# Optimization experiments

Measured on AMD Instinct MI355X. Metric: run time of the kernel, lower is better.

Reference implementation:

```python
import jax, jax.numpy as jnp
import numpy as np

B, C, H, W = 16, 64, 64, 64
MID = max(1, C // 8)


def setup_inputs() -> dict:
    key = jax.random.key(0)
    k1, k2, k3, k4, k5 = jax.random.split(key, 5)
    x = jax.random.normal(k1, (B, C, H, W), dtype=jnp.float32)
    # 1x1 conv weights (spectral-norm conv collapses to a plain [out,in] matrix
    # with a scalar-normalized weight; we use the effective weight directly)
    Wq = jax.random.normal(k2, (MID, C), dtype=jnp.float32) * 0.05
    Wk = jax.random.normal(k3, (MID, C), dtype=jnp.float32) * 0.05
    Wv = jax.random.normal(k4, (C, C), dtype=jnp.float32) * 0.05
    gamma = jax.random.normal(k5, (1,), dtype=jnp.float32) * 0.1
    return {"x": x, "Wq": Wq, "Wk": Wk, "Wv": Wv, "gamma": gamma}


def reference(x, Wq, Wk, Wv, gamma):
    b, c, h, w = x.shape
    n = h * w
    mid = Wq.shape[0]
    xf = x.reshape(b, c, n)                      # [B,C,N]
    q = jnp.einsum('mc,bcn->bnm', Wq, xf)        # [B,N,mid]
    k = jnp.einsum('mc,bcn->bmn', Wk, xf)        # [B,mid,N]
    scale = np.float32(1.0 / np.sqrt(mid))       # torch: / q.size(-1)**0.5, q last dim = mid
    attn = jax.nn.softmax(jnp.einsum('bnm,bmk->bnk', q, k) * scale, axis=-1)  # [B,N,N]
    v = jnp.einsum('oc,bcn->bon', Wv, xf)        # [B,C,N]
    # torch: bmm(v, attn^T) -> out[b,c,j] = sum_n v[b,c,n] * attn[b,j,n]
    out = jnp.einsum('bon,bjn->boj', v, attn).reshape(b, c, h, w)
    return gamma * out + x
```

## Files before the change

### kernel.cpp

```cpp
#include <hip/hip_runtime.h>
#include <hip/hip_bf16.h>

#define BATCH 16
#define CC    64
#define NN    4096
#define MIDD  8

typedef __attribute__((ext_vector_type(8)))  short short8;
typedef __attribute__((ext_vector_type(16))) float f32x16;
typedef __attribute__((ext_vector_type(2)))  int   v2i;

static __device__ __forceinline__ ushort f2bf(float f) {
    return __bfloat16_as_ushort(__float2bfloat16(f));
}

static __device__ __forceinline__ void glds16(const void* g, void* l) {
    __builtin_amdgcn_global_load_lds(
        (const __attribute__((address_space(1))) unsigned int*)g,
        (__attribute__((address_space(3))) unsigned int*)l, 16, 0, 0);
}

static __device__ __forceinline__ unsigned cvt_pk(float lo, float hi) {
    unsigned r;
    asm("v_cvt_pk_bf16_f32 %0, %1, %2" : "=v"(r) : "v"(lo), "v"(hi));
    return r;
}

__global__ __launch_bounds__(256) void proj_kernel(
    const float* __restrict__ x,
    const float* __restrict__ Wq,
    const float* __restrict__ Wk,
    const float* __restrict__ Wv,
    ushort* __restrict__ qtr,
    ushort* __restrict__ ktr,
    ushort* __restrict__ v)
{
    __shared__ unsigned xT[64 * 32];

    int tid = threadIdx.x;
    int b   = blockIdx.x >> 6;
    int n0  = (blockIdx.x & 63) * 64;

    {
        int n  = tid & 63;
        int cp = tid >> 6;
        const float* xb = x + (size_t)b * CC * NN + n0 + n;
#pragma unroll
        for (int rep = 0; rep < 8; ++rep) {
            int c = cp * 2 + rep * 8;
            float a0 = xb[(size_t)c * NN];
            float a1 = xb[(size_t)(c + 1) * NN];
            int dwlog = cp + rep * 4;
            xT[n * 32 + (dwlog ^ (n & 31))] = cvt_pk(a0, a1);
        }
    }

    int wv   = tid >> 6;
    int lane = tid & 63;
    int hi   = lane >> 5;
    int r    = lane & 31;
    int s_   = wv & 1;
    bool hiT = wv >= 2;

    short8 wfa[4], wfb[4];
    if (!hiT) {
        const float* r0 = (r < 8)  ? (Wq + r * 64)
                        : (r < 16) ? (Wk + (r - 8) * 64)
                                   : (Wv + (r - 16) * 64);
        const float* r1 = Wv + (16 + r) * 64;
#pragma unroll
        for (int kc = 0; kc < 4; ++kc) {
            const float4* p0 = (const float4*)(r0 + kc * 16 + hi * 8);
            const float4* p1 = (const float4*)(r1 + kc * 16 + hi * 8);
            float4 a = p0[0], c4 = p0[1];
            float4 e = p1[0], g4 = p1[1];
            union { short8 s8; unsigned u[4]; } wa, wb;
            wa.u[0] = cvt_pk(a.x, a.y);  wa.u[1] = cvt_pk(a.z, a.w);
            wa.u[2] = cvt_pk(c4.x, c4.y); wa.u[3] = cvt_pk(c4.z, c4.w);
            wb.u[0] = cvt_pk(e.x, e.y);  wb.u[1] = cvt_pk(e.z, e.w);
            wb.u[2] = cvt_pk(g4.x, g4.y); wb.u[3] = cvt_pk(g4.z, g4.w);
            wfa[kc] = wa.s8; wfb[kc] = wb.s8;
        }
    } else {
        const float* r2 = Wv + (size_t)(r < 16 ? (48 + r) : 48) * 64;
        short8 z8 = {};
#pragma unroll
        for (int kc = 0; kc < 4; ++kc) {
            const float4* p2 = (const float4*)(r2 + kc * 16 + hi * 8);
            float4 a = p2[0], c4 = p2[1];
            union { short8 s8; unsigned u[4]; } wa;
            wa.u[0] = cvt_pk(a.x, a.y);  wa.u[1] = cvt_pk(a.z, a.w);
            wa.u[2] = cvt_pk(c4.x, c4.y); wa.u[3] = cvt_pk(c4.z, c4.w);
            wfa[kc] = (r < 16) ? wa.s8 : z8;
            wfb[kc] = z8;
        }
    }

    __syncthreads();

    short8 bf[4];
    int nr = s_ * 32 + r;
#pragma unroll
    for (int kc = 0; kc < 4; ++kc) {
        union { short8 s8; unsigned u[4]; } bu;
#pragma unroll
        for (int i = 0; i < 4; ++i) {
            int dwlog = kc * 8 + hi * 4 + i;
            bu.u[i] = xT[nr * 32 + (dwlog ^ r)];
        }
        bf[kc] = bu.s8;
    }

    int ng = n0 + s_ * 32 + r;
    size_t nb = (size_t)b * NN + ng;
    const float SCLQ = 0.35355339059327373f * 1.4426950408889634f;

    if (!hiT) {
        f32x16 acc = {};
#pragma unroll
        for (int kc = 0; kc < 4; ++kc)
            acc = __builtin_amdgcn_mfma_f32_32x32x16_bf16(wfa[kc], bf[kc], acc, 0, 0, 0);
        uint2 qd, kd, zd; zd.x = 0; zd.y = 0;
        qd.x = cvt_pk(acc[0] * SCLQ, acc[1] * SCLQ);
        qd.y = cvt_pk(acc[2] * SCLQ, acc[3] * SCLQ);
        kd.x = cvt_pk(acc[4], acc[5]);
        kd.y = cvt_pk(acc[6], acc[7]);
        *(uint2*)(qtr + nb * 8 + hi * 4) = qd;
        *(uint2*)(ktr + nb * 16 + hi * 4) = kd;
        *(uint2*)(ktr + nb * 16 + 8 + hi * 4) = zd;
#pragma unroll
        for (int reg = 8; reg < 16; ++reg) {
            int ch = (reg & 3) + 8 * ((reg >> 2) - 2) + 4 * hi;
            v[((size_t)b * CC + ch) * NN + ng] = f2bf(acc[reg]);
        }
        f32x16 ac1 = {};
#pragma unroll
        for (int kc = 0; kc < 4; ++kc)
            ac1 = __builtin_amdgcn_mfma_f32_32x32x16_bf16(wfb[kc], bf[kc], ac1, 0, 0, 0);
#pragma unroll
        for (int reg = 0; reg < 16; ++reg) {
            int ch = 16 + (reg & 3) + 8 * (reg >> 2) + 4 * hi;
            v[((size_t)b * CC + ch) * NN + ng] = f2bf(ac1[reg]);
        }
    } else {
        f32x16 acc = {};
#pragma unroll
        for (int kc = 0; kc < 4; ++kc)
            acc = __builtin_amdgcn_mfma_f32_32x32x16_bf16(wfa[kc], bf[kc], acc, 0, 0, 0);
#pragma unroll
        for (int reg = 0; reg < 8; ++reg) {
            int ch = 48 + (reg & 3) + 8 * (reg >> 2) + 4 * hi;
            v[((size_t)b * CC + ch) * NN + ng] = f2bf(acc[reg]);
        }
    }
}

__global__ __launch_bounds__(512, 4) void attn_kernel(
    const ushort* __restrict__ qtr,
    const ushort* __restrict__ ktr,
    const ushort* __restrict__ v,
    const float*  __restrict__ x,
    const float*  __restrict__ gamma,
    float* __restrict__ out)
{
    __shared__ __align__(16) char lds[2 * 3 * 10240];

    int bid = blockIdx.x;
    int wg  = (bid & 7) * 64 + (bid >> 3);
    int b   = wg >> 5;
    int qt  = wg & 31;

    int tid  = threadIdx.x;
    int wv   = tid >> 6;
    int qs   = wv & 3;
    int h    = wv >> 2;
    int lane = tid & 63;
    int hi   = lane >> 5;
    int ql   = lane & 31;
    int q0   = qt * 128 + qs * 32;
    int gt   = tid & 255;

    short8 qf = *(const short8*)(qtr + ((size_t)b * NN + q0 + ql) * 8);
    float  gm = gamma[0];
    short8 zero8 = {};
    if (hi) qf = zero8;
    asm volatile("s_waitcnt vmcnt(0)" ::: "memory");

    const ushort* kbh = ktr + (size_t)b * NN * 16 + (size_t)h * 2048 * 16;
    const ushort* vbh = v   + (size_t)b * CC * NN + h * 2048;

    int oA = gt >> 3, sA = (gt & 7) ^ (oA & 7);
    int oB = oA + 32,  sB = (gt & 7) ^ (oB & 7);
    const ushort* vsrcA = vbh + (size_t)oA * NN + sA * 8;
    const ushort* vsrcB = vbh + (size_t)oB * NN + sB * 8;
    int lk = gt ^ ((gt >> 3) & 7);
    const ushort* ksrc0 = kbh + (size_t)(lk >> 1) * 16 + (lk & 1) * 8;

    char* base = lds + h * 30720;
    int vdA = gt * 16, vdB = (gt + 256) * 16, kd_ = 8192 + gt * 16;
    char* b0 = base;
    char* b1 = base + 10240;
    char* b2 = base + 20480;

    int L0 = ql * 2 + hi;
    int L1 = (32 + ql) * 2 + hi;
    int k0off = 8192 + (L0 ^ ((L0 >> 3) & 7)) * 16;
    int k1off = 8192 + (L1 ^ ((L1 >> 3) & 7)) * 16;

    union { short8 s8; ushort us[8]; } onesu;
#pragma unroll
    for (int i = 0; i < 8; ++i) onesu.us[i] = 0x3F80;
    short8 ones = onesu.s8;

    f32x16 zf   = {};
    f32x16 acc0 = {};
    f32x16 acc1 = {};
    f32x16 accl = {};

    glds16(vsrcA, b0 + vdA); glds16(vsrcB, b0 + vdB);
    if (gt < 128) glds16(ksrc0, b0 + kd_);
    glds16(vsrcA + 64, b1 + vdA); glds16(vsrcB + 64, b1 + vdB);
    if (gt < 128) glds16(ksrc0 + 64 * 16, b1 + kd_);

    for (int t = 0; t < 32; ++t) {
        int k2 = ((t + 2) & 31) * 64;

        __builtin_amdgcn_s_barrier();
        glds16(vsrcA + k2, b2 + vdA);
        glds16(vsrcB + k2, b2 + vdB);
        if (gt < 128) {
            glds16(ksrc0 + (size_t)k2 * 16, b2 + kd_);
            asm volatile("s_waitcnt vmcnt(6)" ::: "memory");
        } else {
            asm volatile("s_waitcnt vmcnt(4)" ::: "memory");
        }
        __builtin_amdgcn_s_barrier();
        __builtin_amdgcn_sched_barrier(0);

#pragma unroll
        for (int c = 0; c < 2; ++c) {
            short8 kf = *(const short8*)(b0 + (c ? k1off : k0off));
            f32x16 s = __builtin_amdgcn_mfma_f32_32x32x16_bf16(kf, qf, zf, 0, 0, 0);

            float p[16];
#pragma unroll
            for (int r = 0; r < 16; ++r) p[r] = __builtin_amdgcn_exp2f(s[r]);

            unsigned u[8];
#pragma unroll
            for (int i = 0; i < 8; ++i) u[i] = cvt_pk(p[2 * i], p[2 * i + 1]);

            v2i r02 = __builtin_amdgcn_permlane32_swap(u[0], u[2], false, false);
            v2i r13 = __builtin_amdgcn_permlane32_swap(u[1], u[3], false, false);
            v2i r46 = __builtin_amdgcn_permlane32_swap(u[4], u[6], false, false);
            v2i r57 = __builtin_amdgcn_permlane32_swap(u[5], u[7], false, false);
            union { short8 s8; int i4[4]; } P0, P1;
            P0.i4[0] = r02.x; P0.i4[1] = r13.x; P0.i4[2] = r02.y; P0.i4[3] = r13.y;
            P1.i4[0] = r46.x; P1.i4[1] = r57.x; P1.i4[2] = r46.y; P1.i4[3] = r57.y;

            int g0 = (ql * 8 + ((c * 4 + hi) ^ (ql & 7))) * 16;
            int g1 = (ql * 8 + ((c * 4 + 2 + hi) ^ (ql & 7))) * 16;
            short8 vA0 = *(const short8*)(b0 + g0);
            short8 vB0 = *(const short8*)(b0 + g0 + 4096);
            short8 vA1 = *(const short8*)(b0 + g1);
            short8 vB1 = *(const short8*)(b0 + g1 + 4096);

            __builtin_amdgcn_s_setprio(1);
            acc0 = __builtin_amdgcn_mfma_f32_32x32x16_bf16(vA0, P0.s8, acc0, 0, 0, 0);
            acc1 = __builtin_amdgcn_mfma_f32_32x32x16_bf16(vB0, P0.s8, acc1, 0, 0, 0);
            accl = __builtin_amdgcn_mfma_f32_32x32x16_bf16(ones, P0.s8, accl, 0, 0, 0);
            acc0 = __builtin_amdgcn_mfma_f32_32x32x16_bf16(vA1, P1.s8, acc0, 0, 0, 0);
            acc1 = __builtin_amdgcn_mfma_f32_32x32x16_bf16(vB1, P1.s8, acc1, 0, 0, 0);
            accl = __builtin_amdgcn_mfma_f32_32x32x16_bf16(ones, P1.s8, accl, 0, 0, 0);
            __builtin_amdgcn_s_setprio(0);
        }

        char* tp = b0; b0 = b1; b1 = b2; b2 = tp;
    }

    asm volatile("s_waitcnt vmcnt(0)" ::: "memory");
    __syncthreads();

    float* cl = (float*)lds;
    if (h == 1) {
#pragma unroll
        for (int r = 0; r < 16; ++r) {
            int ch = (r & 3) + 8 * (r >> 2) + 4 * hi;
            cl[(qs * 64 + ch) * 32 + ql]      = acc0[r];
            cl[(qs * 64 + 32 + ch) * 32 + ql] = acc1[r];
        }
        cl[8192 + qs * 32 + ql] = accl[0];
    }
    __syncthreads();
    if (h == 0) {
        float den = accl[0] + cl[8192 + qs * 32 + ql];
        float inv = gm / den;
#pragma unroll
        for (int r = 0; r < 16; ++r) {
            int ch = (r & 3) + 8 * (r >> 2) + 4 * hi;
            float n0 = acc0[r] + cl[(qs * 64 + ch) * 32 + ql];
            float n1 = acc1[r] + cl[(qs * 64 + 32 + ch) * 32 + ql];
            size_t i0 = ((size_t)(b * CC + ch)) * NN + q0 + ql;
            size_t i1 = i0 + (size_t)32 * NN;
            out[i0] = n0 * inv + x[i0];
            out[i1] = n1 * inv + x[i1];
        }
    }
}

extern "C" void kernel_launch(void* const* d_in, const int* in_sizes, int n_in,
                              void* d_out, int out_size, void* d_ws, size_t ws_size,
                              hipStream_t stream) {
    const float* x     = (const float*)d_in[0];
    const float* Wq    = (const float*)d_in[1];
    const float* Wk    = (const float*)d_in[2];
    const float* Wv    = (const float*)d_in[3];
    const float* gamma = (const float*)d_in[4];
    float* out = (float*)d_out;

    ushort* qtr = (ushort*)d_ws;
    ushort* ktr = qtr + (size_t)BATCH * NN * 8;
    ushort* vws = ktr + (size_t)BATCH * NN * 16;

    proj_kernel<<<dim3((BATCH * NN) / 64), dim3(256), 0, stream>>>(x, Wq, Wk, Wv, qtr, ktr, vws);
    attn_kernel<<<dim3((BATCH * NN) / 128), dim3(512), 0, stream>>>(qtr, ktr, vws, x, gamma, out);
}
```

Baseline: 142.4 us.

## Shrink attention blocks to 64 queries with double buffering; loop projection over two tiles

The attention kernel now uses 256-thread blocks covering 64 queries each, twice as many blocks, and double-buffers K/V in LDS instead of triple-buffering. This cuts LDS per block, which should allow more resident blocks. The cost is that each K/V tile now feeds only 2 query waves per half, so global/L2 traffic for K/V roughly doubles, and the prefetch distance drops to one tile. The projection kernel now processes two 64-column tiles per block, reusing the converted weight fragments and halving its block count.

```diff
diff --git a/kernel.cpp b/kernel.cpp
--- a/kernel.cpp
+++ b/kernel.cpp
@@ -38,22 +38,8 @@
     __shared__ unsigned xT[64 * 32];
 
     int tid = threadIdx.x;
-    int b   = blockIdx.x >> 6;
-    int n0  = (blockIdx.x & 63) * 64;
-
-    {
-        int n  = tid & 63;
-        int cp = tid >> 6;
-        const float* xb = x + (size_t)b * CC * NN + n0 + n;
-#pragma unroll
-        for (int rep = 0; rep < 8; ++rep) {
-            int c = cp * 2 + rep * 8;
-            float a0 = xb[(size_t)c * NN];
-            float a1 = xb[(size_t)(c + 1) * NN];
-            int dwlog = cp + rep * 4;
-            xT[n * 32 + (dwlog ^ (n & 31))] = cvt_pk(a0, a1);
-        }
-    }
+    int b   = blockIdx.x >> 5;
+    int c0  = (blockIdx.x & 31) * 128;
 
     int wv   = tid >> 6;
     int lane = tid & 63;
@@ -96,66 +82,84 @@
         }
     }
 
-    __syncthreads();
-
-    short8 bf[4];
-    int nr = s_ * 32 + r;
-#pragma unroll
-    for (int kc = 0; kc < 4; ++kc) {
-        union { short8 s8; unsigned u[4]; } bu;
-#pragma unroll
-        for (int i = 0; i < 4; ++i) {
-            int dwlog = kc * 8 + hi * 4 + i;
-            bu.u[i] = xT[nr * 32 + (dwlog ^ r)];
-        }
-        bf[kc] = bu.s8;
-    }
-
-    int ng = n0 + s_ * 32 + r;
-    size_t nb = (size_t)b * NN + ng;
+    int ns = tid & 63;
+    int cp = tid >> 6;
     const float SCLQ = 0.35355339059327373f * 1.4426950408889634f;
 
-    if (!hiT) {
-        f32x16 acc = {};
-#pragma unroll
-        for (int kc = 0; kc < 4; ++kc)
-            acc = __builtin_amdgcn_mfma_f32_32x32x16_bf16(wfa[kc], bf[kc], acc, 0, 0, 0);
-        uint2 qd, kd, zd; zd.x = 0; zd.y = 0;
-        qd.x = cvt_pk(acc[0] * SCLQ, acc[1] * SCLQ);
-        qd.y = cvt_pk(acc[2] * SCLQ, acc[3] * SCLQ);
-        kd.x = cvt_pk(acc[4], acc[5]);
-        kd.y = cvt_pk(acc[6], acc[7]);
-        *(uint2*)(qtr + nb * 8 + hi * 4) = qd;
-        *(uint2*)(ktr + nb * 16 + hi * 4) = kd;
-        *(uint2*)(ktr + nb * 16 + 8 + hi * 4) = zd;
-#pragma unroll
-        for (int reg = 8; reg < 16; ++reg) {
-            int ch = (reg & 3) + 8 * ((reg >> 2) - 2) + 4 * hi;
-            v[((size_t)b * CC + ch) * NN + ng] = f2bf(acc[reg]);
-        }
-        f32x16 ac1 = {};
-#pragma unroll
-        for (int kc = 0; kc < 4; ++kc)
-            ac1 = __builtin_amdgcn_mfma_f32_32x32x16_bf16(wfb[kc], bf[kc], ac1, 0, 0, 0);
-#pragma unroll
-        for (int reg = 0; reg < 16; ++reg) {
-            int ch = 16 + (reg & 3) + 8 * (reg >> 2) + 4 * hi;
-            v[((size_t)b * CC + ch) * NN + ng] = f2bf(ac1[reg]);
-        }
-    } else {
-        f32x16 acc = {};
-#pragma unroll
-        for (int kc = 0; kc < 4; ++kc)
-            acc = __builtin_amdgcn_mfma_f32_32x32x16_bf16(wfa[kc], bf[kc], acc, 0, 0, 0);
-#pragma unroll
-        for (int reg = 0; reg < 8; ++reg) {
-            int ch = 48 + (reg & 3) + 8 * (reg >> 2) + 4 * hi;
-            v[((size_t)b * CC + ch) * NN + ng] = f2bf(acc[reg]);
-        }
-    }
-}
-
-__global__ __launch_bounds__(512, 4) void attn_kernel(
+    for (int it = 0; it < 2; ++it) {
+        int n0 = c0 + it * 64;
+        __syncthreads();
+        {
+            const float* xb = x + (size_t)b * CC * NN + n0 + ns;
+#pragma unroll
+            for (int rep = 0; rep < 8; ++rep) {
+                int c = cp * 2 + rep * 8;
+                float a0 = xb[(size_t)c * NN];
+                float a1 = xb[(size_t)(c + 1) * NN];
+                int dwlog = cp + rep * 4;
+                xT[ns * 32 + (dwlog ^ (ns & 31))] = cvt_pk(a0, a1);
+            }
+        }
+        __syncthreads();
+
+        short8 bf[4];
+        int nr = s_ * 32 + r;
+#pragma unroll
+        for (int kc = 0; kc < 4; ++kc) {
+            union { short8 s8; unsigned u[4]; } bu;
+#pragma unroll
+            for (int i = 0; i < 4; ++i) {
+                int dwlog = kc * 8 + hi * 4 + i;
+                bu.u[i] = xT[nr * 32 + (dwlog ^ r)];
+            }
+            bf[kc] = bu.s8;
+        }
+
+        int ng = n0 + s_ * 32 + r;
+        size_t nb = (size_t)b * NN + ng;
+
+        if (!hiT) {
+            f32x16 acc = {};
+#pragma unroll
+            for (int kc = 0; kc < 4; ++kc)
+                acc = __builtin_amdgcn_mfma_f32_32x32x16_bf16(wfa[kc], bf[kc], acc, 0, 0, 0);
+            uint2 qd, kd, zd; zd.x = 0; zd.y = 0;
+            qd.x = cvt_pk(acc[0] * SCLQ, acc[1] * SCLQ);
+            qd.y = cvt_pk(acc[2] * SCLQ, acc[3] * SCLQ);
+            kd.x = cvt_pk(acc[4], acc[5]);
+            kd.y = cvt_pk(acc[6], acc[7]);
+            *(uint2*)(qtr + nb * 8 + hi * 4) = qd;
+            *(uint2*)(ktr + nb * 16 + hi * 4) = kd;
+            *(uint2*)(ktr + nb * 16 + 8 + hi * 4) = zd;
+#pragma unroll
+            for (int reg = 8; reg < 16; ++reg) {
+                int ch = (reg & 3) + 8 * ((reg >> 2) - 2) + 4 * hi;
+                v[((size_t)b * CC + ch) * NN + ng] = f2bf(acc[reg]);
+            }
+            f32x16 ac1 = {};
+#pragma unroll
+            for (int kc = 0; kc < 4; ++kc)
+                ac1 = __builtin_amdgcn_mfma_f32_32x32x16_bf16(wfb[kc], bf[kc], ac1, 0, 0, 0);
+#pragma unroll
+            for (int reg = 0; reg < 16; ++reg) {
+                int ch = 16 + (reg & 3) + 8 * (reg >> 2) + 4 * hi;
+                v[((size_t)b * CC + ch) * NN + ng] = f2bf(ac1[reg]);
+            }
+        } else {
+            f32x16 acc = {};
+#pragma unroll
+            for (int kc = 0; kc < 4; ++kc)
+                acc = __builtin_amdgcn_mfma_f32_32x32x16_bf16(wfa[kc], bf[kc], acc, 0, 0, 0);
+#pragma unroll
+            for (int reg = 0; reg < 8; ++reg) {
+                int ch = 48 + (reg & 3) + 8 * (reg >> 2) + 4 * hi;
+                v[((size_t)b * CC + ch) * NN + ng] = f2bf(acc[reg]);
+            }
+        }
+    }
+}
+
+__global__ __launch_bounds__(256, 4) void attn_kernel(
     const ushort* __restrict__ qtr,
     const ushort* __restrict__ ktr,
     const ushort* __restrict__ v,
@@ -163,22 +167,21 @@
     const float*  __restrict__ gamma,
     float* __restrict__ out)
 {
-    __shared__ __align__(16) char lds[2 * 3 * 10240];
+    __shared__ __align__(16) char lds[2 * 2 * 10240];
 
     int bid = blockIdx.x;
-    int wg  = (bid & 7) * 64 + (bid >> 3);
-    int b   = wg >> 5;
-    int qt  = wg & 31;
+    int wg  = (bid & 7) * 128 + (bid >> 3);
+    int b   = wg >> 6;
+    int qt  = wg & 63;
 
     int tid  = threadIdx.x;
-    int wv   = tid >> 6;
-    int qs   = wv & 3;
-    int h    = wv >> 2;
+    int h    = tid >> 7;
+    int gt   = tid & 127;
+    int qs   = (tid >> 6) & 1;
     int lane = tid & 63;
     int hi   = lane >> 5;
     int ql   = lane & 31;
-    int q0   = qt * 128 + qs * 32;
-    int gt   = tid & 255;
+    int q0   = qt * 64 + qs * 32;
 
     short8 qf = *(const short8*)(qtr + ((size_t)b * NN + q0 + ql) * 8);
     float  gm = gamma[0];
@@ -189,18 +192,23 @@
     const ushort* kbh = ktr + (size_t)b * NN * 16 + (size_t)h * 2048 * 16;
     const ushort* vbh = v   + (size_t)b * CC * NN + h * 2048;
 
-    int oA = gt >> 3, sA = (gt & 7) ^ (oA & 7);
-    int oB = oA + 32,  sB = (gt & 7) ^ (oB & 7);
-    const ushort* vsrcA = vbh + (size_t)oA * NN + sA * 8;
-    const ushort* vsrcB = vbh + (size_t)oB * NN + sB * 8;
+    const ushort* vsrc[4];
+    int vd[4];
+#pragma unroll
+    for (int j = 0; j < 4; ++j) {
+        int g  = gt + j * 128;
+        int o  = g >> 3;
+        int sl = (g & 7) ^ (o & 7);
+        vsrc[j] = vbh + (size_t)o * NN + sl * 8;
+        vd[j]   = g * 16;
+    }
     int lk = gt ^ ((gt >> 3) & 7);
-    const ushort* ksrc0 = kbh + (size_t)(lk >> 1) * 16 + (lk & 1) * 8;
-
-    char* base = lds + h * 30720;
-    int vdA = gt * 16, vdB = (gt + 256) * 16, kd_ = 8192 + gt * 16;
-    char* b0 = base;
-    char* b1 = base + 10240;
-    char* b2 = base + 20480;
+    const ushort* ksrc = kbh + (size_t)(lk >> 1) * 16 + (lk & 1) * 8;
+    int kd = 8192 + gt * 16;
+
+    char* base = lds + h * 20480;
+    char* cur  = base;
+    char* nxt  = base + 10240;
 
     int L0 = ql * 2 + hi;
     int L1 = (32 + ql) * 2 + hi;
@@ -217,29 +225,24 @@
     f32x16 acc1 = {};
     f32x16 accl = {};
 
-    glds16(vsrcA, b0 + vdA); glds16(vsrcB, b0 + vdB);
-    if (gt < 128) glds16(ksrc0, b0 + kd_);
-    glds16(vsrcA + 64, b1 + vdA); glds16(vsrcB + 64, b1 + vdB);
-    if (gt < 128) glds16(ksrc0 + 64 * 16, b1 + kd_);
+#pragma unroll
+    for (int j = 0; j < 4; ++j) glds16(vsrc[j], cur + vd[j]);
+    glds16(ksrc, cur + kd);
 
     for (int t = 0; t < 32; ++t) {
-        int k2 = ((t + 2) & 31) * 64;
+        int k1 = ((t + 1) & 31) * 64;
 
         __builtin_amdgcn_s_barrier();
-        glds16(vsrcA + k2, b2 + vdA);
-        glds16(vsrcB + k2, b2 + vdB);
-        if (gt < 128) {
-            glds16(ksrc0 + (size_t)k2 * 16, b2 + kd_);
-            asm volatile("s_waitcnt vmcnt(6)" ::: "memory");
-        } else {
-            asm volatile("s_waitcnt vmcnt(4)" ::: "memory");
-        }
+#pragma unroll
+        for (int j = 0; j < 4; ++j) glds16(vsrc[j] + k1, nxt + vd[j]);
+        glds16(ksrc + (size_t)k1 * 16, nxt + kd);
+        asm volatile("s_waitcnt vmcnt(5)" ::: "memory");
         __builtin_amdgcn_s_barrier();
         __builtin_amdgcn_sched_barrier(0);
 
 #pragma unroll
         for (int c = 0; c < 2; ++c) {
-            short8 kf = *(const short8*)(b0 + (c ? k1off : k0off));
+            short8 kf = *(const short8*)(cur + (c ? k1off : k0off));
             f32x16 s = __builtin_amdgcn_mfma_f32_32x32x16_bf16(kf, qf, zf, 0, 0, 0);
 
             float p[16];
@@ -260,10 +263,10 @@
 
             int g0 = (ql * 8 + ((c * 4 + hi) ^ (ql & 7))) * 16;
             int g1 = (ql * 8 + ((c * 4 + 2 + hi) ^ (ql & 7))) * 16;
-            short8 vA0 = *(const short8*)(b0 + g0);
-            short8 vB0 = *(const short8*)(b0 + g0 + 4096);
-            short8 vA1 = *(const short8*)(b0 + g1);
-            short8 vB1 = *(const short8*)(b0 + g1 + 4096);
+            short8 vA0 = *(const short8*)(cur + g0);
+            short8 vB0 = *(const short8*)(cur + g0 + 4096);
+            short8 vA1 = *(const short8*)(cur + g1);
+            short8 vB1 = *(const short8*)(cur + g1 + 4096);
 
             __builtin_amdgcn_s_setprio(1);
             acc0 = __builtin_amdgcn_mfma_f32_32x32x16_bf16(vA0, P0.s8, acc0, 0, 0, 0);
@@ -275,7 +278,7 @@
             __builtin_amdgcn_s_setprio(0);
         }
 
-        char* tp = b0; b0 = b1; b1 = b2; b2 = tp;
+        char* tp = cur; cur = nxt; nxt = tp;
     }
 
     asm volatile("s_waitcnt vmcnt(0)" ::: "memory");
@@ -289,11 +292,11 @@
             cl[(qs * 64 + ch) * 32 + ql]      = acc0[r];
             cl[(qs * 64 + 32 + ch) * 32 + ql] = acc1[r];
         }
-        cl[8192 + qs * 32 + ql] = accl[0];
+        cl[4096 + qs * 32 + ql] = accl[0];
     }
     __syncthreads();
     if (h == 0) {
-        float den = accl[0] + cl[8192 + qs * 32 + ql];
+        float den = accl[0] + cl[4096 + qs * 32 + ql];
         float inv = gm / den;
 #pragma unroll
         for (int r = 0; r < 16; ++r) {
@@ -322,6 +325,6 @@
     ushort* ktr = qtr + (size_t)BATCH * NN * 8;
     ushort* vws = ktr + (size_t)BATCH * NN * 16;
 
-    proj_kernel<<<dim3((BATCH * NN) / 64), dim3(256), 0, stream>>>(x, Wq, Wk, Wv, qtr, ktr, vws);
-    attn_kernel<<<dim3((BATCH * NN) / 128), dim3(512), 0, stream>>>(qtr, ktr, vws, x, gamma, out);
-}
+    proj_kernel<<<dim3(BATCH * 32), dim3(256), 0, stream>>>(x, Wq, Wk, Wv, qtr, ktr, vws);
+    attn_kernel<<<dim3(BATCH * 64), dim3(256), 0, stream>>>(qtr, ktr, vws, x, gamma, out);
+}
```

Result: no change. 142.1 us (-0.2%).
